# Optimization experiments

Hardware: AMD Instinct MI355X
Metric: run time of the kernel (lower is better)

## Reference

```python
import jax, jax.numpy as jnp
import numpy as np

B, L, D, H = 2, 2048, 1024, 16
d = D // H  # head dim = 64


def setup_inputs() -> dict:
    key = jax.random.key(0)
    ks = jax.random.split(key, 6)
    X = jax.random.normal(ks[0], (B, L, D), dtype=jnp.float32)
    scale = 0.02
    Wq = scale * jax.random.normal(ks[1], (D, D), dtype=jnp.float32)
    Wk = scale * jax.random.normal(ks[2], (D, D), dtype=jnp.float32)
    Wv = scale * jax.random.normal(ks[3], (D, D), dtype=jnp.float32)
    Wc = scale * jax.random.normal(ks[4], (D, D), dtype=jnp.float32)
    Ltri = scale * jax.random.normal(ks[5], (H, d, d), dtype=jnp.float32)
    return {"X": X, "Wq": Wq, "Wk": Wk, "Wv": Wv, "Wc": Wc, "Ltri": Ltri}


def reference(X, Wq, Wk, Wv, Wc, Ltri):
    # torch nn.Linear: y = x @ W.T (bias=False); dropout is identity in eval.
    Bsz, Lq, Dm = X.shape
    Q = (X @ Wq.T).reshape(Bsz, Lq, H, d)
    K = (X @ Wk.T).reshape(Bsz, Lq, H, d)
    V = (X @ Wv.T).reshape(Bsz, Lq, H, d)
    # Causal linear attention: cumulative sum of per-position K outer V.
    # W[b,l,h,:,:] = sum_{t<=l} K[b,t,h,:] outer V[b,t,h,:]
    KV = jnp.einsum('blhd,blhe->blhde', K, V)  # [B,L,H,d,d]
    KVc = jnp.cumsum(KV, axis=1)
    Y = jnp.einsum('blhd,blhde->blhe', Q, KVc)  # [B,L,H,d]
    # Learned SPD head-mixing matrix Bm = Lm @ Lm.T with Lm lower-triangular.
    mask = jnp.tril(jnp.ones((1, d, d), dtype=X.dtype))
    Lm = Ltri * mask  # [H,d,d]
    Bm = Lm @ jnp.swapaxes(Lm, -2, -1)  # [H,d,d]
    Y = jnp.einsum('hed,blhd->blhe', Bm, Y)
    Y = Y.reshape(Bsz, Lq, Dm)
    return Y @ Wc.T
```

## Files before the change

kernel.cpp:

```cpp
#include <hip/hip_runtime.h>


#define DEV static __device__ __forceinline__

typedef unsigned short u16;
typedef unsigned long long u64;
typedef __attribute__((ext_vector_type(4))) float f32x4;
typedef __attribute__((ext_vector_type(8))) short bf16x8;

DEV u16 f2bf(float f){
  union { float f; unsigned u; } v; v.f = f;
  unsigned r = v.u + 0x7FFFu + ((v.u >> 16) & 1u);
  return (u16)(r >> 16);
}

DEV void store_val(float* p, float v){ *p = v; }
DEV void store_val(u16* p, float v){ *p = f2bf(v); }

DEV void gload16(const void* g, void* l){
  __builtin_amdgcn_global_load_lds((const __attribute__((address_space(1))) void*)g,
                                   (__attribute__((address_space(3))) void*)l, 16, 0, 0);
}

__global__ __launch_bounds__(256) void prep_kernel(
    const float* __restrict__ X, u16* __restrict__ Xb,
    const float* __restrict__ Wq, u16* __restrict__ Wqb,
    const float* __restrict__ Wk, u16* __restrict__ Wkb,
    const float* __restrict__ Wv, u16* __restrict__ Wvb,
    const float* __restrict__ Wc, u16* __restrict__ Wcb,
    const float* __restrict__ Ltri, u16* __restrict__ Bmb)
{
  const int bx = blockIdx.x, tid = threadIdx.x;
  if(bx < 16){
    __shared__ float Lm[64][65];
    int h = bx;
    const float* src = Ltri + (size_t)h * 4096;
    for(int i = tid; i < 4096; i += 256){
      int e = i >> 6, k = i & 63;
      Lm[e][k] = (k <= e) ? src[i] : 0.f;
    }
    __syncthreads();
    u16* out = Bmb + (size_t)h * 4096;
    for(int i = tid; i < 4096; i += 256){
      int e = i >> 6, dk = i & 63;
      float sum = 0.f;
      int kmax = e < dk ? e : dk;
      for(int k = 0; k <= kmax; k++) sum += Lm[e][k] * Lm[dk][k];
      out[i] = f2bf(sum);
    }
  } else {
    const int n0 = 4194304, n1 = 1048576, n2 = 1048576, n3 = 1048576, n4 = 1048576;
    int total = (n0 + n1 + n2 + n3 + n4) >> 2;
    for(int i = (bx - 16) * 256 + tid; i < total; i += 2048 * 256){
      int e = i << 2;
      const float* s; u16* d;
      if(e < n0){ s = X + e; d = Xb + e; }
      else if(e < n0 + n1){ s = Wq + (e - n0); d = Wqb + (e - n0); }
      else if(e < n0 + n1 + n2){ s = Wk + (e - n0 - n1); d = Wkb + (e - n0 - n1); }
      else if(e < n0 + n1 + n2 + n3){ s = Wv + (e - n0 - n1 - n2); d = Wvb + (e - n0 - n1 - n2); }
      else { s = Wc + (e - n0 - n1 - n2 - n3); d = Wcb + (e - n0 - n1 - n2 - n3); }
      float4 v = *(const float4*)s;
      u64 pk = (u64)f2bf(v.x) | ((u64)f2bf(v.y) << 16) | ((u64)f2bf(v.z) << 32) | ((u64)f2bf(v.w) << 48);
      *(u64*)d = pk;
    }
  }
}

template<typename OutT>
DEV void gemm128_p2(const u16* __restrict__ A, const u16* __restrict__ W,
                    OutT* __restrict__ C, int bx, int by, int N, int K)
{
  __shared__ u16 L[3][8192];
  const int tid = threadIdx.x;
  const int wid = tid >> 6, lane = tid & 63;
  const int wr = wid >> 1, wc = wid & 1;
  const int lr = lane & 15, lq = lane >> 4;
  const u16* Ag = A + (size_t)(bx * 128) * K;
  const u16* Wg = W + (size_t)(by * 128) * K;

  const int p0 = tid >> 3, p1 = 32 + (tid >> 3);
  const int cl0 = (tid & 7) ^ (p0 & 7);
  const int cl1 = (tid & 7) ^ (p1 & 7);
  const int srow0 = 2 * p0 + (cl0 >> 2), skc0 = (cl0 & 3) * 8;
  const int srow1 = 2 * p1 + (cl1 >> 2), skc1 = (cl1 & 3) * 8;

  auto stagef = [&](int kt, int buf){
    gload16(Ag + (size_t)srow0 * K + kt * 32 + skc0, &L[buf][tid * 8]);
    gload16(Ag + (size_t)srow1 * K + kt * 32 + skc1, &L[buf][2048 + tid * 8]);
    gload16(Wg + (size_t)srow0 * K + kt * 32 + skc0, &L[buf][4096 + tid * 8]);
    gload16(Wg + (size_t)srow1 * K + kt * 32 + skc1, &L[buf][6144 + tid * 8]);
  };

  const int nt = K >> 5;
  f32x4 acc[4][4] = {};
  stagef(0, 0);
  stagef(1, 1);
  int cur = 0;
  for(int t = 0; t < nt; t++){
    if(t < nt - 1) asm volatile("s_waitcnt vmcnt(4)" ::: "memory");
    else           asm volatile("s_waitcnt vmcnt(0)" ::: "memory");
    __builtin_amdgcn_s_barrier();
    __builtin_amdgcn_sched_barrier(0);
    if(t + 2 < nt){
      int n2 = cur >= 1 ? cur - 1 : cur + 2;
      stagef(t + 2, n2);
    }
    const u16* Lb = L[cur];
    bf16x8 af[4], bfr[4];
#pragma unroll
    for(int i = 0; i < 4; i++){
      int row = wr * 64 + i * 16 + lr;
      int rh = row >> 1;
      int cph = (lq | ((row & 1) << 2)) ^ (rh & 7);
      af[i] = *(const bf16x8*)&Lb[rh * 64 + cph * 8];
    }
#pragma unroll
    for(int j = 0; j < 4; j++){
      int row = wc * 64 + j * 16 + lr;
      int rh = row >> 1;
      int cph = (lq | ((row & 1) << 2)) ^ (rh & 7);
      bfr[j] = *(const bf16x8*)&Lb[4096 + rh * 64 + cph * 8];
    }
#pragma unroll
    for(int i = 0; i < 4; i++)
#pragma unroll
      for(int j = 0; j < 4; j++)
        acc[i][j] = __builtin_amdgcn_mfma_f32_16x16x32_bf16(af[i], bfr[j], acc[i][j], 0, 0, 0);
    cur = cur == 2 ? 0 : cur + 1;
  }
#pragma unroll
  for(int i = 0; i < 4; i++)
#pragma unroll
    for(int j = 0; j < 4; j++)
#pragma unroll
      for(int r = 0; r < 4; r++){
        int row = bx * 128 + wr * 64 + i * 16 + (lane >> 4) * 4 + r;
        int col = by * 128 + wc * 64 + j * 16 + lr;
        store_val(C + (size_t)row * N + col, acc[i][j][r]);
      }
}

__global__ __launch_bounds__(256) void qkv_gemm(
    const u16* __restrict__ Xb,
    const u16* __restrict__ Wq, const u16* __restrict__ Wk, const u16* __restrict__ Wv,
    u16* __restrict__ Q, u16* __restrict__ Ko, u16* __restrict__ V,
    const u16* __restrict__ Wcb, const u16* __restrict__ Bmb, u16* __restrict__ Wcpb)
{
  if(blockIdx.y >= 24){
    int rt = blockIdx.x & 7, h = (blockIdx.x >> 3) + ((blockIdx.y - 24) << 2);
    int wid = threadIdx.x >> 6, lane = threadIdx.x & 63;
    int lr = lane & 15, lk8 = (lane >> 4) * 8, lq = lane >> 4;
    const u16* ab  = Wcb + (size_t)(rt * 128) * 1024 + h * 64;
    const u16* bm  = Bmb + (size_t)h * 4096;
    f32x4 acc[2][4] = {};
#pragma unroll
    for(int i = 0; i < 2; i++){
      int mf = wid * 2 + i;
#pragma unroll
      for(int ks = 0; ks < 2; ks++){
        bf16x8 a = *(const bf16x8*)(ab + (size_t)(mf * 16 + lr) * 1024 + ks * 32 + lk8);
#pragma unroll
        for(int nf = 0; nf < 4; nf++){
          bf16x8 bfr = *(const bf16x8*)(bm + (nf * 16 + lr) * 64 + ks * 32 + lk8);
          acc[i][nf] = __builtin_amdgcn_mfma_f32_16x16x32_bf16(a, bfr, acc[i][nf], 0, 0, 0);
        }
      }
    }
#pragma unroll
    for(int i = 0; i < 2; i++)
#pragma unroll
      for(int nf = 0; nf < 4; nf++)
#pragma unroll
        for(int r = 0; r < 4; r++){
          int row = rt * 128 + (wid * 2 + i) * 16 + lq * 4 + r;
          int col = h * 64 + nf * 16 + lr;
          Wcpb[(size_t)row * 1024 + col] = f2bf(acc[i][nf][r]);
        }
    return;
  }
  int sel = blockIdx.y >> 3, byl = blockIdx.y & 7;
  const u16* W = sel == 0 ? Wq : sel == 1 ? Wk : Wv;
  u16* C = sel == 0 ? Q : sel == 1 ? Ko : V;
  gemm128_p2<u16>(Xb, W, C, blockIdx.x, byl, 1024, 1024);
}

__global__ __launch_bounds__(256) void out_gemm(
    const u16* __restrict__ Yb, const u16* __restrict__ Wcpb, float* __restrict__ out)
{
  gemm128_p2<float>(Yb, Wcpb, out, blockIdx.x, blockIdx.y, 1024, 1024);
}

__global__ __launch_bounds__(256) void state_chunk(
    const u16* __restrict__ Kb, const u16* __restrict__ Vb,
    u16* __restrict__ VT, float* __restrict__ Sc)
{
  int bh = blockIdx.x, c = blockIdx.y;
  int b = bh >> 4, h = bh & 15;
  int tid = threadIdx.x;
  __shared__ u16 Kt[128][72];
  __shared__ u16 Vt[128][72];
  int rr = tid >> 3;
  int cc = (tid & 7) * 8;
  const u16* kg = Kb + (size_t)(b * 2048 + c * 128) * 1024 + h * 64;
  const u16* vg = Vb + (size_t)(b * 2048 + c * 128) * 1024 + h * 64;
#pragma unroll
  for(int p = 0; p < 4; p++){
    int row = rr + p * 32;
    *(int4*)&Kt[row][cc] = *(const int4*)(kg + (size_t)row * 1024 + cc);
    *(int4*)&Vt[row][cc] = *(const int4*)(vg + (size_t)row * 1024 + cc);
  }
  __syncthreads();
  {
    int d = tid >> 2, tseg = (tid & 3) * 32;
    u16* vto = VT + (size_t)bh * 64 * 2048 + (size_t)d * 2048 + c * 128 + tseg;
#pragma unroll
    for(int j = 0; j < 32; j += 8){
      u16 tmp[8] __attribute__((aligned(16)));
#pragma unroll
      for(int q = 0; q < 8; q++) tmp[q] = Vt[tseg + j + q][d];
      *(int4*)(vto + j) = *(const int4*)tmp;
    }
  }
  int wid = tid >> 6, lane = tid & 63;
  int wr = wid >> 1, wc = wid & 1;
  int lr = lane & 15, lk8 = (lane >> 4) * 8, lq = lane >> 4;
  f32x4 acc[2][2] = {};
#pragma unroll
  for(int ks = 0; ks < 4; ks++){
    bf16x8 a[2], bb[2];
#pragma unroll
    for(int i = 0; i < 2; i++){
      u16 tmp[8] __attribute__((aligned(16)));
      int e = wr * 32 + i * 16 + lr;
#pragma unroll
      for(int q = 0; q < 8; q++) tmp[q] = Vt[ks * 32 + lk8 + q][e];
      a[i] = *(const bf16x8*)tmp;
    }
#pragma unroll
    for(int j = 0; j < 2; j++){
      u16 tmp[8] __attribute__((aligned(16)));
      int dk = wc * 32 + j * 16 + lr;
#pragma unroll
      for(int q = 0; q < 8; q++) tmp[q] = Kt[ks * 32 + lk8 + q][dk];
      bb[j] = *(const bf16x8*)tmp;
    }
#pragma unroll
    for(int i = 0; i < 2; i++)
#pragma unroll
      for(int j = 0; j < 2; j++)
        acc[i][j] = __builtin_amdgcn_mfma_f32_16x16x32_bf16(a[i], bb[j], acc[i][j], 0, 0, 0);
  }
  float* out = Sc + ((size_t)bh * 16 + c) * 4096;
#pragma unroll
  for(int i = 0; i < 2; i++)
#pragma unroll
    for(int j = 0; j < 2; j++)
#pragma unroll
      for(int r = 0; r < 4; r++){
        int e = wr * 32 + i * 16 + lq * 4 + r, dk = wc * 32 + j * 16 + lr;
        out[e * 64 + dk] = acc[i][j][r];
      }
}

__global__ __launch_bounds__(256) void prefix_state(const float* __restrict__ Sc, u16* __restrict__ Scb)
{
  int bh = blockIdx.x >> 2, part = blockIdx.x & 3;
  int e4 = part * 256 + threadIdx.x;
  const float4* s = (const float4*)(Sc + (size_t)bh * 65536) + e4;
  u16* d = Scb + (size_t)bh * 65536 + e4 * 4;
  float4 run = {0.f, 0.f, 0.f, 0.f};
  for(int c = 0; c < 16; c++){
    float4 v = s[(size_t)c * 1024];
    u64 pk = (u64)f2bf(run.x) | ((u64)f2bf(run.y) << 16) | ((u64)f2bf(run.z) << 32) | ((u64)f2bf(run.w) << 48);
    *(u64*)(d + (size_t)c * 4096) = pk;
    run.x += v.x; run.y += v.y; run.z += v.z; run.w += v.w;
  }
}

__global__ __launch_bounds__(256) void chunk_attn(
    const u16* __restrict__ Q, const u16* __restrict__ Kmat,
    const u16* __restrict__ VT, const u16* __restrict__ Scb, u16* __restrict__ Y)
{
  int bh = blockIdx.x, c = blockIdx.y;
  int b = bh >> 4, h = bh & 15;
  int t = threadIdx.x, wid = t >> 6, lane = t & 63;
  int lr = lane & 15, lk8 = (lane >> 4) * 8, lq = lane >> 4;
  __shared__ u16 S[128 * 128];
  const u16* qg = Q    + (size_t)(b * 2048 + c * 128) * 1024 + h * 64;
  const u16* kg = Kmat + (size_t)(b * 2048 + c * 128) * 1024 + h * 64;
  const u16* scb = Scb + ((size_t)bh * 16 + c) * 4096;
  const u16* vt  = VT + (size_t)bh * 64 * 2048 + (size_t)c * 128;
  u16* yg = Y + (size_t)(b * 2048 + c * 128) * 1024 + h * 64;
#pragma unroll
  for(int mi = 0; mi < 2; mi++){
    int mf = wid + mi * 4;
    int Rm = mf * 16;
    if((mf & 1) == 0){
      int zr = Rm + (lane >> 2), zc = Rm + 16 + (lane & 3) * 4;
      int zoff = ((zr * 128 + zc) * 2) ^ ((zr & 7) << 4);
      *(u64*)((char*)S + zoff) = 0ULL;
    }
    bf16x8 a[2];
#pragma unroll
    for(int ks = 0; ks < 2; ks++) a[ks] = *(const bf16x8*)(qg + (size_t)(Rm + lr) * 1024 + ks * 32 + lk8);
    for(int nf = 0; nf <= mf; nf++){
      f32x4 acc = {};
#pragma unroll
      for(int ks = 0; ks < 2; ks++){
        bf16x8 bb = *(const bf16x8*)(kg + (size_t)(nf * 16 + lr) * 1024 + ks * 32 + lk8);
        acc = __builtin_amdgcn_mfma_f32_16x16x32_bf16(a[ks], bb, acc, 0, 0, 0);
      }
#pragma unroll
      for(int r = 0; r < 4; r++){
        int row = lq * 4 + r, col = lr;
        float v = acc[r];
        if(nf == mf && col > row) v = 0.f;
        int grow = Rm + row, gcol = nf * 16 + col;
        int off = ((grow * 128 + gcol) * 2) ^ ((grow & 7) << 4);
        *(u16*)((char*)S + off) = f2bf(v);
      }
    }
    f32x4 acc2[4] = {};
#pragma unroll
    for(int nf = 0; nf < 4; nf++){
#pragma unroll
      for(int ks = 0; ks < 2; ks++){
        bf16x8 bb = *(const bf16x8*)(scb + (nf * 16 + lr) * 64 + ks * 32 + lk8);
        acc2[nf] = __builtin_amdgcn_mfma_f32_16x16x32_bf16(a[ks], bb, acc2[nf], 0, 0, 0);
      }
    }
    int ksmax = mf >> 1;
    for(int ks = 0; ks <= ksmax; ks++){
      int row = Rm + lr;
      int off = ((row * 128 + ks * 32 + lk8) * 2) ^ ((row & 7) << 4);
      bf16x8 af = *(const bf16x8*)((char*)S + off);
#pragma unroll
      for(int nf = 0; nf < 4; nf++){
        bf16x8 bb = *(const bf16x8*)(vt + (size_t)(nf * 16 + lr) * 2048 + ks * 32 + lk8);
        acc2[nf] = __builtin_amdgcn_mfma_f32_16x16x32_bf16(af, bb, acc2[nf], 0, 0, 0);
      }
    }
#pragma unroll
    for(int nf = 0; nf < 4; nf++)
#pragma unroll
      for(int r = 0; r < 4; r++){
        int grow = Rm + lq * 4 + r, gcol = nf * 16 + lr;
        yg[(size_t)grow * 1024 + gcol] = f2bf(acc2[nf][r]);
      }
  }
}

extern "C" void kernel_launch(void* const* d_in, const int* in_sizes, int n_in,
                              void* d_out, int out_size, void* d_ws, size_t ws_size,
                              hipStream_t stream)
{
  const float* X    = (const float*)d_in[0];
  const float* Wq   = (const float*)d_in[1];
  const float* Wk   = (const float*)d_in[2];
  const float* Wv   = (const float*)d_in[3];
  const float* Wc   = (const float*)d_in[4];
  const float* Ltri = (const float*)d_in[5];
  float* out = (float*)d_out;

  char* ws = (char*)d_ws;
  size_t off = 0;
  auto carve = [&](size_t bytes) -> char* {
    char* p = ws + off;
    off += (bytes + 255) & ~(size_t)255;
    return p;
  };
  u16* Xb   = (u16*)carve((size_t)4194304 * 2);
  u16* Wqb  = (u16*)carve((size_t)1048576 * 2);
  u16* Wkb  = (u16*)carve((size_t)1048576 * 2);
  u16* Wvb  = (u16*)carve((size_t)1048576 * 2);
  u16* Wcb  = (u16*)carve((size_t)1048576 * 2);
  u16* Wcpb = (u16*)carve((size_t)1048576 * 2);
  u16* Bmb  = (u16*)carve((size_t)65536 * 2);
  u16* Qb   = (u16*)carve((size_t)4194304 * 2);
  u16* Kb   = (u16*)carve((size_t)4194304 * 2);
  u16* Vb   = (u16*)carve((size_t)4194304 * 2);
  u16* VT   = (u16*)carve((size_t)4194304 * 2);
  float* Sc = (float*)carve((size_t)2097152 * 4);
  u16* Scb  = (u16*)carve((size_t)2097152 * 2);
  u16* Yb   = (u16*)carve((size_t)4194304 * 2);
  (void)in_sizes; (void)n_in; (void)out_size; (void)ws_size;

  prep_kernel<<<2064, 256, 0, stream>>>(X, Xb, Wq, Wqb, Wk, Wkb, Wv, Wvb, Wc, Wcb, Ltri, Bmb);
  qkv_gemm<<<dim3(32, 28), 256, 0, stream>>>(Xb, Wqb, Wkb, Wvb, Qb, Kb, Vb, Wcb, Bmb, Wcpb);
  state_chunk<<<dim3(32, 16), 256, 0, stream>>>(Kb, Vb, VT, Sc);
  prefix_state<<<128, 256, 0, stream>>>(Sc, Scb);
  chunk_attn<<<dim3(32, 16), 256, 0, stream>>>(Qb, Kb, VT, Scb, Yb);
  out_gemm<<<dim3(32, 8), 256, 0, stream>>>(Yb, Wcpb, out);
}
```

Before: 105.1 us.

## Replace QKV GEMM with 256x256-tile, 8-wave, LDS-pipelined kernel over fused weights

Replaces the 128x128 QKV projection GEMM with one 512-thread kernel that computes 256x256 output tiles over a concatenated Wq/Wk/Wv weight (passed as Wqb, which relies on contiguous workspace carving). It uses double-buffered async global-to-LDS loads split into quarter stages, interleaved with MFMA phases, with s_setprio and a swizzled tile order. The Wc·Bm side computation is folded into the tail blocks, each handling two sub-tiles. The aim is more data reuse per LDS load and better overlap of loads with math. In exchange it uses 128KB of LDS per block, which limits occupancy, and adds fragile barrier and waitcnt choreography.

```diff
diff --git a/kernel.cpp b/kernel.cpp
--- a/kernel.cpp
+++ b/kernel.cpp
@@ -66,6 +66,202 @@
   }
 }
 
+DEV bf16x8 ldsf(const u16* buf, int row, int kc){
+  return *(const bf16x8*)(buf + row * 64 + ((kc ^ (row & 7)) * 8));
+}
+DEV void stageA(const u16* At, u16* bufA, int tid){
+#pragma unroll
+  for(int l = 0; l < 2; l++){
+    int r = l * 128 + (tid >> 3);
+    int c = tid & 7;
+    gload16(At + (size_t)r * 1024 + (c ^ (r & 7)) * 8, bufA + r * 64 + c * 8);
+  }
+}
+DEV void stageA1(const u16* At, u16* bufA, int tid){
+#pragma unroll
+  for(int l = 0; l < 2; l++){
+    int r = 64 + l * 128 + (tid >> 3);
+    int c = tid & 7;
+    gload16(At + (size_t)r * 1024 + (c ^ (r & 7)) * 8, bufA + r * 64 + c * 8);
+  }
+}
+DEV void stageB(const u16* Wt, u16* bufB, int tid, int qn){
+#pragma unroll
+  for(int l = 0; l < 2; l++){
+    int rr = l * 64 + (tid >> 3);
+    int r = (rr >> 5) * 64 + qn * 32 + (rr & 31);
+    int c = tid & 7;
+    gload16(Wt + (size_t)r * 1024 + (c ^ (r & 7)) * 8, bufB + r * 64 + c * 8);
+  }
+}
+
+__global__ __launch_bounds__(512, 2) void qkv8_gemm(
+    const u16* __restrict__ Xb, const u16* __restrict__ Wall,
+    u16* __restrict__ QKV,
+    const u16* __restrict__ Wcb, const u16* __restrict__ Bmb, u16* __restrict__ Wcpb)
+{
+  if(blockIdx.x >= 192){
+    int ob = (blockIdx.x - 192) * 2 + (threadIdx.x >> 8);
+    int t = threadIdx.x & 255;
+    int rt = ob & 7, h = ob >> 3;
+    int lane = t & 63, wid = t >> 6;
+    int lr = lane & 15, lk8 = (lane >> 4) * 8, lq = lane >> 4;
+    const u16* ab  = Wcb + (size_t)(rt * 128) * 1024 + h * 64;
+    const u16* bm  = Bmb + (size_t)h * 4096;
+    f32x4 acc[2][4] = {};
+#pragma unroll
+    for(int i = 0; i < 2; i++){
+      int mf = wid * 2 + i;
+#pragma unroll
+      for(int ks = 0; ks < 2; ks++){
+        bf16x8 a = *(const bf16x8*)(ab + (size_t)(mf * 16 + lr) * 1024 + ks * 32 + lk8);
+#pragma unroll
+        for(int nf = 0; nf < 4; nf++){
+          bf16x8 bfr = *(const bf16x8*)(bm + (nf * 16 + lr) * 64 + ks * 32 + lk8);
+          acc[i][nf] = __builtin_amdgcn_mfma_f32_16x16x32_bf16(a, bfr, acc[i][nf], 0, 0, 0);
+        }
+      }
+    }
+#pragma unroll
+    for(int i = 0; i < 2; i++)
+#pragma unroll
+      for(int nf = 0; nf < 4; nf++)
+#pragma unroll
+        for(int r = 0; r < 4; r++){
+          int row = rt * 128 + (wid * 2 + i) * 16 + lq * 4 + r;
+          int col = h * 64 + nf * 16 + lr;
+          Wcpb[(size_t)row * 1024 + col] = f2bf(acc[i][nf][r]);
+        }
+    return;
+  }
+
+  __shared__ u16 Lds[65536];
+  const int tid = threadIdx.x;
+  const int wid = tid >> 6, lane = tid & 63;
+  const int wm = wid >> 2, wn = wid & 3;
+  const int lr = lane & 15, lq = lane >> 4;
+  int tix = blockIdx.x;
+  int tix2 = (tix & 7) * 24 + (tix >> 3);
+  int bxg = tix2 & 15, byg = tix2 >> 4;
+  const u16* Ab = Xb   + (size_t)(bxg * 256) * 1024;
+  const u16* Wb = Wall + (size_t)(byg * 256) * 1024;
+
+  f32x4 acc[8][4] = {};
+  bf16x8 af[4][2], b0[2][2], b1[2][2];
+  const int nt = 16;
+
+  stageA (Ab, Lds, tid);
+  stageA1(Ab, Lds, tid);
+  stageB (Wb, Lds + 16384, tid, 0);
+  stageB (Wb, Lds + 16384, tid, 1);
+  stageA (Ab + 64, Lds + 32768, tid);
+  stageB (Wb + 64, Lds + 32768 + 16384, tid, 0);
+  asm volatile("s_waitcnt vmcnt(4)" ::: "memory");
+  __builtin_amdgcn_s_barrier();
+
+  for(int t = 0; t < nt; t++){
+    u16* bufA = Lds + (t & 1) * 32768;  u16* bufB = bufA + 16384;
+    u16* oA   = Lds + ((t & 1) ^ 1) * 32768;  u16* oB = oA + 16384;
+
+#pragma unroll
+    for(int i = 0; i < 4; i++)
+#pragma unroll
+      for(int ks = 0; ks < 2; ks++)
+        af[i][ks] = ldsf(bufA, wm * 128 + i * 16 + lr, ks * 4 + lq);
+#pragma unroll
+    for(int j = 0; j < 2; j++)
+#pragma unroll
+      for(int ks = 0; ks < 2; ks++)
+        b0[j][ks] = ldsf(bufB, wn * 64 + j * 16 + lr, ks * 4 + lq);
+    if(t + 1 < nt) stageA1(Ab + (t + 1) * 64, oA, tid);
+    __builtin_amdgcn_s_barrier();
+    asm volatile("s_waitcnt lgkmcnt(0)" ::: "memory");
+    __builtin_amdgcn_sched_barrier(0);
+    __builtin_amdgcn_s_setprio(1);
+#pragma unroll
+    for(int i = 0; i < 4; i++)
+#pragma unroll
+      for(int j = 0; j < 2; j++)
+#pragma unroll
+        for(int ks = 0; ks < 2; ks++)
+          acc[i][j] = __builtin_amdgcn_mfma_f32_16x16x32_bf16(af[i][ks], b0[j][ks], acc[i][j], 0, 0, 0);
+    __builtin_amdgcn_s_setprio(0);
+    __builtin_amdgcn_s_barrier();
+
+#pragma unroll
+    for(int j = 0; j < 2; j++)
+#pragma unroll
+      for(int ks = 0; ks < 2; ks++)
+        b1[j][ks] = ldsf(bufB, wn * 64 + 32 + j * 16 + lr, ks * 4 + lq);
+    if(t + 1 < nt) stageB(Wb + (t + 1) * 64, oB, tid, 1);
+    __builtin_amdgcn_s_barrier();
+    asm volatile("s_waitcnt lgkmcnt(0)" ::: "memory");
+    __builtin_amdgcn_sched_barrier(0);
+    __builtin_amdgcn_s_setprio(1);
+#pragma unroll
+    for(int i = 0; i < 4; i++)
+#pragma unroll
+      for(int j = 0; j < 2; j++)
+#pragma unroll
+        for(int ks = 0; ks < 2; ks++)
+          acc[i][2 + j] = __builtin_amdgcn_mfma_f32_16x16x32_bf16(af[i][ks], b1[j][ks], acc[i][2 + j], 0, 0, 0);
+    __builtin_amdgcn_s_setprio(0);
+    __builtin_amdgcn_s_barrier();
+
+#pragma unroll
+    for(int i = 0; i < 4; i++)
+#pragma unroll
+      for(int ks = 0; ks < 2; ks++)
+        af[i][ks] = ldsf(bufA, wm * 128 + 64 + i * 16 + lr, ks * 4 + lq);
+    if(t + 2 < nt) stageA(Ab + (t + 2) * 64, bufA, tid);
+    __builtin_amdgcn_s_barrier();
+    asm volatile("s_waitcnt lgkmcnt(0)" ::: "memory");
+    __builtin_amdgcn_sched_barrier(0);
+    __builtin_amdgcn_s_setprio(1);
+#pragma unroll
+    for(int i = 0; i < 4; i++)
+#pragma unroll
+      for(int j = 0; j < 2; j++)
+#pragma unroll
+        for(int ks = 0; ks < 2; ks++)
+          acc[4 + i][j] = __builtin_amdgcn_mfma_f32_16x16x32_bf16(af[i][ks], b0[j][ks], acc[4 + i][j], 0, 0, 0);
+    __builtin_amdgcn_s_setprio(0);
+    __builtin_amdgcn_s_barrier();
+
+    if(t + 2 < nt) stageB(Wb + (t + 2) * 64, bufB, tid, 0);
+    asm volatile("s_waitcnt vmcnt(4)" ::: "memory");
+    __builtin_amdgcn_s_barrier();
+    __builtin_amdgcn_s_setprio(1);
+#pragma unroll
+    for(int i = 0; i < 4; i++)
+#pragma unroll
+      for(int j = 0; j < 2; j++)
+#pragma unroll
+        for(int ks = 0; ks < 2; ks++)
+          acc[4 + i][2 + j] = __builtin_amdgcn_mfma_f32_16x16x32_bf16(af[i][ks], b1[j][ks], acc[4 + i][2 + j], 0, 0, 0);
+    __builtin_amdgcn_s_setprio(0);
+    __builtin_amdgcn_s_barrier();
+  }
+
+  int col0 = byg * 256;
+  u16* dst = QKV + (size_t)(col0 >> 10) * 4194304;
+  int colin0 = col0 & 1023;
+#pragma unroll
+  for(int qm = 0; qm < 2; qm++)
+#pragma unroll
+    for(int i = 0; i < 4; i++)
+#pragma unroll
+      for(int qn = 0; qn < 2; qn++)
+#pragma unroll
+        for(int j = 0; j < 2; j++)
+#pragma unroll
+          for(int r = 0; r < 4; r++){
+            int row = bxg * 256 + wm * 128 + qm * 64 + i * 16 + lq * 4 + r;
+            int col = colin0 + wn * 64 + qn * 32 + j * 16 + lr;
+            dst[(size_t)row * 1024 + col] = f2bf(acc[qm * 4 + i][qn * 2 + j][r]);
+          }
+}
+
 template<typename OutT>
 DEV void gemm128_p2(const u16* __restrict__ A, const u16* __restrict__ W,
                     OutT* __restrict__ C, int bx, int by, int N, int K)
@@ -138,50 +334,6 @@
         int col = by * 128 + wc * 64 + j * 16 + lr;
         store_val(C + (size_t)row * N + col, acc[i][j][r]);
       }
-}
-
-__global__ __launch_bounds__(256) void qkv_gemm(
-    const u16* __restrict__ Xb,
-    const u16* __restrict__ Wq, const u16* __restrict__ Wk, const u16* __restrict__ Wv,
-    u16* __restrict__ Q, u16* __restrict__ Ko, u16* __restrict__ V,
-    const u16* __restrict__ Wcb, const u16* __restrict__ Bmb, u16* __restrict__ Wcpb)
-{
-  if(blockIdx.y >= 24){
-    int rt = blockIdx.x & 7, h = (blockIdx.x >> 3) + ((blockIdx.y - 24) << 2);
-    int wid = threadIdx.x >> 6, lane = threadIdx.x & 63;
-    int lr = lane & 15, lk8 = (lane >> 4) * 8, lq = lane >> 4;
-    const u16* ab  = Wcb + (size_t)(rt * 128) * 1024 + h * 64;
-    const u16* bm  = Bmb + (size_t)h * 4096;
-    f32x4 acc[2][4] = {};
-#pragma unroll
-    for(int i = 0; i < 2; i++){
-      int mf = wid * 2 + i;
-#pragma unroll
-      for(int ks = 0; ks < 2; ks++){
-        bf16x8 a = *(const bf16x8*)(ab + (size_t)(mf * 16 + lr) * 1024 + ks * 32 + lk8);
-#pragma unroll
-        for(int nf = 0; nf < 4; nf++){
-          bf16x8 bfr = *(const bf16x8*)(bm + (nf * 16 + lr) * 64 + ks * 32 + lk8);
-          acc[i][nf] = __builtin_amdgcn_mfma_f32_16x16x32_bf16(a, bfr, acc[i][nf], 0, 0, 0);
-        }
-      }
-    }
-#pragma unroll
-    for(int i = 0; i < 2; i++)
-#pragma unroll
-      for(int nf = 0; nf < 4; nf++)
-#pragma unroll
-        for(int r = 0; r < 4; r++){
-          int row = rt * 128 + (wid * 2 + i) * 16 + lq * 4 + r;
-          int col = h * 64 + nf * 16 + lr;
-          Wcpb[(size_t)row * 1024 + col] = f2bf(acc[i][nf][r]);
-        }
-    return;
-  }
-  int sel = blockIdx.y >> 3, byl = blockIdx.y & 7;
-  const u16* W = sel == 0 ? Wq : sel == 1 ? Wk : Wv;
-  u16* C = sel == 0 ? Q : sel == 1 ? Ko : V;
-  gemm128_p2<u16>(Xb, W, C, blockIdx.x, byl, 1024, 1024);
 }
 
 __global__ __launch_bounds__(256) void out_gemm(
@@ -386,7 +538,7 @@
   (void)in_sizes; (void)n_in; (void)out_size; (void)ws_size;
 
   prep_kernel<<<2064, 256, 0, stream>>>(X, Xb, Wq, Wqb, Wk, Wkb, Wv, Wvb, Wc, Wcb, Ltri, Bmb);
-  qkv_gemm<<<dim3(32, 28), 256, 0, stream>>>(Xb, Wqb, Wkb, Wvb, Qb, Kb, Vb, Wcb, Bmb, Wcpb);
+  qkv8_gemm<<<256, 512, 0, stream>>>(Xb, Wqb, Qb, Wcb, Bmb, Wcpb);
   state_chunk<<<dim3(32, 16), 256, 0, stream>>>(Kb, Vb, VT, Sc);
   prefix_state<<<128, 256, 0, stream>>>(Sc, Scb);
   chunk_attn<<<dim3(32, 16), 256, 0, stream>>>(Qb, Kb, VT, Scb, Yb);
```

Measured after the change: 104.2 us. About the same (-0.8%).

## Swizzle GEMM block IDs across XCDs and share V loads in chunk attention

Applied to the files above, without the earlier changes.

The QKV and output GEMMs now remap the linear block id as (id&7)*N + id>>3. Blocks that run on the same XCD (assuming round-robin dispatch) then cover neighbouring tiles and can share operands in that XCD's L2. In chunk_attn, each wave keeps both of its Q row-tiles in registers and runs the state-product and intra-chunk S·V stages for both tiles in one loop. Each V^T fragment load is then reused for two MFMA row-tiles instead of being reloaded. The cost is more live registers, which may lower occupancy.

```diff
diff --git a/kernel.cpp b/kernel.cpp
--- a/kernel.cpp
+++ b/kernel.cpp
@@ -178,16 +178,21 @@
         }
     return;
   }
-  int sel = blockIdx.y >> 3, byl = blockIdx.y & 7;
+  int id = blockIdx.y * 32 + blockIdx.x;
+  int id2 = (id & 7) * 96 + (id >> 3);
+  int bxg = id2 & 31, byg = id2 >> 5;
+  int sel = byg >> 3, byl = byg & 7;
   const u16* W = sel == 0 ? Wq : sel == 1 ? Wk : Wv;
   u16* C = sel == 0 ? Q : sel == 1 ? Ko : V;
-  gemm128_p2<u16>(Xb, W, C, blockIdx.x, byl, 1024, 1024);
+  gemm128_p2<u16>(Xb, W, C, bxg, byl, 1024, 1024);
 }
 
 __global__ __launch_bounds__(256) void out_gemm(
     const u16* __restrict__ Yb, const u16* __restrict__ Wcpb, float* __restrict__ out)
 {
-  gemm128_p2<float>(Yb, Wcpb, out, blockIdx.x, blockIdx.y, 1024, 1024);
+  int id = blockIdx.y * 32 + blockIdx.x;
+  int id2 = (id & 7) * 32 + (id >> 3);
+  gemm128_p2<float>(Yb, Wcpb, out, id2 & 31, id2 >> 5, 1024, 1024);
 }
 
 __global__ __launch_bounds__(256) void state_chunk(
@@ -291,6 +296,8 @@
   const u16* scb = Scb + ((size_t)bh * 16 + c) * 4096;
   const u16* vt  = VT + (size_t)bh * 64 * 2048 + (size_t)c * 128;
   u16* yg = Y + (size_t)(b * 2048 + c * 128) * 1024 + h * 64;
+
+  bf16x8 a[2][2];
 #pragma unroll
   for(int mi = 0; mi < 2; mi++){
     int mf = wid + mi * 4;
@@ -300,15 +307,14 @@
       int zoff = ((zr * 128 + zc) * 2) ^ ((zr & 7) << 4);
       *(u64*)((char*)S + zoff) = 0ULL;
     }
-    bf16x8 a[2];
-#pragma unroll
-    for(int ks = 0; ks < 2; ks++) a[ks] = *(const bf16x8*)(qg + (size_t)(Rm + lr) * 1024 + ks * 32 + lk8);
+#pragma unroll
+    for(int ks = 0; ks < 2; ks++) a[mi][ks] = *(const bf16x8*)(qg + (size_t)(Rm + lr) * 1024 + ks * 32 + lk8);
     for(int nf = 0; nf <= mf; nf++){
       f32x4 acc = {};
 #pragma unroll
       for(int ks = 0; ks < 2; ks++){
         bf16x8 bb = *(const bf16x8*)(kg + (size_t)(nf * 16 + lr) * 1024 + ks * 32 + lk8);
-        acc = __builtin_amdgcn_mfma_f32_16x16x32_bf16(a[ks], bb, acc, 0, 0, 0);
+        acc = __builtin_amdgcn_mfma_f32_16x16x32_bf16(a[mi][ks], bb, acc, 0, 0, 0);
       }
 #pragma unroll
       for(int r = 0; r < 4; r++){
@@ -320,32 +326,49 @@
         *(u16*)((char*)S + off) = f2bf(v);
       }
     }
-    f32x4 acc2[4] = {};
-#pragma unroll
-    for(int nf = 0; nf < 4; nf++){
-#pragma unroll
-      for(int ks = 0; ks < 2; ks++){
-        bf16x8 bb = *(const bf16x8*)(scb + (nf * 16 + lr) * 64 + ks * 32 + lk8);
-        acc2[nf] = __builtin_amdgcn_mfma_f32_16x16x32_bf16(a[ks], bb, acc2[nf], 0, 0, 0);
-      }
-    }
-    int ksmax = mf >> 1;
-    for(int ks = 0; ks <= ksmax; ks++){
-      int row = Rm + lr;
-      int off = ((row * 128 + ks * 32 + lk8) * 2) ^ ((row & 7) << 4);
+  }
+  f32x4 acc2[2][4] = {};
+#pragma unroll
+  for(int nf = 0; nf < 4; nf++)
+#pragma unroll
+    for(int ks = 0; ks < 2; ks++){
+      bf16x8 bb = *(const bf16x8*)(scb + (nf * 16 + lr) * 64 + ks * 32 + lk8);
+#pragma unroll
+      for(int mi = 0; mi < 2; mi++)
+        acc2[mi][nf] = __builtin_amdgcn_mfma_f32_16x16x32_bf16(a[mi][ks], bb, acc2[mi][nf], 0, 0, 0);
+    }
+  int ks0 = wid >> 1;
+  int row0 = wid * 16 + lr;
+  int row1 = (wid + 4) * 16 + lr;
+  for(int ks = 0; ks <= ks0 + 2; ks++){
+    bf16x8 bb[4];
+#pragma unroll
+    for(int nf = 0; nf < 4; nf++)
+      bb[nf] = *(const bf16x8*)(vt + (size_t)(nf * 16 + lr) * 2048 + ks * 32 + lk8);
+    if(ks <= ks0){
+      int off = ((row0 * 128 + ks * 32 + lk8) * 2) ^ ((row0 & 7) << 4);
       bf16x8 af = *(const bf16x8*)((char*)S + off);
 #pragma unroll
-      for(int nf = 0; nf < 4; nf++){
-        bf16x8 bb = *(const bf16x8*)(vt + (size_t)(nf * 16 + lr) * 2048 + ks * 32 + lk8);
-        acc2[nf] = __builtin_amdgcn_mfma_f32_16x16x32_bf16(af, bb, acc2[nf], 0, 0, 0);
-      }
-    }
+      for(int nf = 0; nf < 4; nf++)
+        acc2[0][nf] = __builtin_amdgcn_mfma_f32_16x16x32_bf16(af, bb[nf], acc2[0][nf], 0, 0, 0);
+    }
+    {
+      int off = ((row1 * 128 + ks * 32 + lk8) * 2) ^ ((row1 & 7) << 4);
+      bf16x8 af = *(const bf16x8*)((char*)S + off);
+#pragma unroll
+      for(int nf = 0; nf < 4; nf++)
+        acc2[1][nf] = __builtin_amdgcn_mfma_f32_16x16x32_bf16(af, bb[nf], acc2[1][nf], 0, 0, 0);
+    }
+  }
+#pragma unroll
+  for(int mi = 0; mi < 2; mi++){
+    int Rm = (wid + mi * 4) * 16;
 #pragma unroll
     for(int nf = 0; nf < 4; nf++)
 #pragma unroll
       for(int r = 0; r < 4; r++){
         int grow = Rm + lq * 4 + r, gcol = nf * 16 + lr;
-        yg[(size_t)grow * 1024 + gcol] = f2bf(acc2[nf][r]);
+        yg[(size_t)grow * 1024 + gcol] = f2bf(acc2[mi][nf][r]);
       }
   }
 }
```

New measurement: 107.8 us. 1.03x slower.
